# Performance work log

Measured on AMD Instinct MI355X. Metric: run time of the kernel, lower is better.

The kernel has to match this reference:

```python
import jax, jax.numpy as jnp
import numpy as np

N = 16384
D = 256


def setup_inputs() -> dict:
    key = jax.random.key(0)
    k1, k2, k3, k4 = jax.random.split(key, 4)
    x = jax.random.normal(k1, (N, D), dtype=jnp.float32)
    adj = jax.random.randint(k2, (N, N), 0, 2, dtype=jnp.int32)  # dense 0/1 adjacency
    W = jax.random.normal(k3, (D, D), dtype=jnp.float32) * 0.05
    b = jax.random.normal(k4, (D,), dtype=jnp.float32) * 0.05
    return {"x": x, "adj": adj, "W": W, "b": b}


def reference(x, adj, W, b):
    # neighbors of node i are columns where adj[i, :] == 1; mean-aggregate then Linear
    a = (adj == 1).astype(x.dtype)               # [N, N]
    deg = jnp.sum(a, axis=1, keepdims=True)      # [N, 1]
    agg = jnp.einsum('ij,jf->if', a, x) / deg    # mean over neighbors, [N, D]
    return agg @ W.T + b                         # nn.Linear(in, out)
```

## Files before the change

kernel.cpp:

```cpp
#include <hip/hip_runtime.h>
#include <stdint.h>

typedef __attribute__((ext_vector_type(8))) short shortx8;
typedef __attribute__((ext_vector_type(4))) float floatx4;

#define NR 16384
#define DD 256
#define SA 72
#define KCH 8192
#define BK 64
#define NIT (KCH / BK)

__device__ __forceinline__ unsigned short f2bf(float f) {
    union { float f; uint32_t u; } v; v.f = f;
    uint32_t u = v.u;
    return (unsigned short)((u + 0x7FFFu + ((u >> 16) & 1u)) >> 16);
}

__global__ __launch_bounds__(256) void k_xpose(const float* __restrict__ x,
                                               unsigned short* __restrict__ xT) {
    __shared__ unsigned short t[64][72];
    const int kb = blockIdx.x * 64;
    const int nb = blockIdx.y * 64;
    const int tid = threadIdx.x;
    const int lr = tid >> 4;
    const int lc = (tid & 15) * 4;
#pragma unroll
    for (int i = 0; i < 4; ++i) {
        const int k = kb + lr + 16 * i;
        const float4 v = *(const float4*)(x + (size_t)k * DD + nb + lc);
        t[lc + 0][lr + 16 * i] = f2bf(v.x);
        t[lc + 1][lr + 16 * i] = f2bf(v.y);
        t[lc + 2][lr + 16 * i] = f2bf(v.z);
        t[lc + 3][lr + 16 * i] = f2bf(v.w);
    }
    __syncthreads();
#pragma unroll
    for (int i = 0; i < 4; ++i) {
        const int nl = lr + 16 * i;
        ushort4 o;
        o.x = t[nl][lc + 0]; o.y = t[nl][lc + 1];
        o.z = t[nl][lc + 2]; o.w = t[nl][lc + 3];
        *(ushort4*)(xT + (size_t)(nb + nl) * NR + kb + lc) = o;
    }
}

__global__ __launch_bounds__(256, 2) void k_agg(const int* __restrict__ adj,
                                                const unsigned short* __restrict__ xT,
                                                float* __restrict__ aggP,
                                                float* __restrict__ degP) {
    __shared__ __align__(16) unsigned short As[64 * SA];
    __shared__ __align__(16) unsigned short Bs[256 * SA];
    __shared__ int degs[64];

    const int tid  = threadIdx.x;
    const int wave = tid >> 6;
    const int lane = tid & 63;
    const int q    = lane >> 4;
    const int ln   = lane & 15;
    const int m0   = blockIdx.x * 64;
    const int kb0  = blockIdx.y * KCH;

    if (tid < 64) degs[tid] = 0;

    const int arow = tid >> 4;
    const int acol = (tid & 15) * 4;

    const int* ap0 = adj + (size_t)(m0 + arow) * NR + kb0 + acol;
    const int* ap1 = ap0 + (size_t)16 * NR;
    const int* ap2 = ap0 + (size_t)32 * NR;
    const int* ap3 = ap0 + (size_t)48 * NR;

    const unsigned short* bg[9];
    unsigned short* const blb = Bs + wave * 9 * 512;
#pragma unroll
    for (int j = 0; j < 9; ++j) {
        const int cid = (wave * 9 + j) * 64 + lane;
        const int n = cid / 9;
        int c = cid - n * 9; if (c > 7) c = 7;
        bg[j] = xT + (size_t)n * NR + kb0 + c * 8;
    }

    floatx4 acc[4][4] = {};
    int dacc0 = 0, dacc1 = 0, dacc2 = 0, dacc3 = 0;

    for (int it = 0; it < NIT; ++it) {
        __syncthreads();

#pragma unroll
        for (int j = 0; j < 9; ++j) {
            __builtin_amdgcn_global_load_lds(
                (const __attribute__((address_space(1))) void*)bg[j],
                (__attribute__((address_space(3))) void*)(blb + j * 512),
                16, 0, 0);
            bg[j] += BK;
        }

        const int4 a0 = *(const int4*)ap0; ap0 += BK;
        const int4 a1 = *(const int4*)ap1; ap1 += BK;
        const int4 a2 = *(const int4*)ap2; ap2 += BK;
        const int4 a3 = *(const int4*)ap3; ap3 += BK;

        ushort4 w;
        w.x = a0.x ? 0x3F80 : 0; w.y = a0.y ? 0x3F80 : 0;
        w.z = a0.z ? 0x3F80 : 0; w.w = a0.w ? 0x3F80 : 0;
        *(ushort4*)&As[(arow +  0) * SA + acol] = w;
        dacc0 += a0.x + a0.y + a0.z + a0.w;

        w.x = a1.x ? 0x3F80 : 0; w.y = a1.y ? 0x3F80 : 0;
        w.z = a1.z ? 0x3F80 : 0; w.w = a1.w ? 0x3F80 : 0;
        *(ushort4*)&As[(arow + 16) * SA + acol] = w;
        dacc1 += a1.x + a1.y + a1.z + a1.w;

        w.x = a2.x ? 0x3F80 : 0; w.y = a2.y ? 0x3F80 : 0;
        w.z = a2.z ? 0x3F80 : 0; w.w = a2.w ? 0x3F80 : 0;
        *(ushort4*)&As[(arow + 32) * SA + acol] = w;
        dacc2 += a2.x + a2.y + a2.z + a2.w;

        w.x = a3.x ? 0x3F80 : 0; w.y = a3.y ? 0x3F80 : 0;
        w.z = a3.z ? 0x3F80 : 0; w.w = a3.w ? 0x3F80 : 0;
        *(ushort4*)&As[(arow + 48) * SA + acol] = w;
        dacc3 += a3.x + a3.y + a3.z + a3.w;

        __syncthreads();

#pragma unroll
        for (int ks = 0; ks < 2; ++ks) {
            const int kk = ks * 32 + q * 8;
            shortx8 af[4], bf[4];
#pragma unroll
            for (int mt = 0; mt < 4; ++mt)
                af[mt] = *(const shortx8*)&As[(mt * 16 + ln) * SA + kk];
#pragma unroll
            for (int nt = 0; nt < 4; ++nt)
                bf[nt] = *(const shortx8*)&Bs[(wave * 64 + nt * 16 + ln) * SA + kk];
#pragma unroll
            for (int mt = 0; mt < 4; ++mt)
#pragma unroll
                for (int nt = 0; nt < 4; ++nt)
                    acc[mt][nt] = __builtin_amdgcn_mfma_f32_16x16x32_bf16(
                        af[mt], bf[nt], acc[mt][nt], 0, 0, 0);
        }
    }

    atomicAdd(&degs[arow +  0], dacc0);
    atomicAdd(&degs[arow + 16], dacc1);
    atomicAdd(&degs[arow + 32], dacc2);
    atomicAdd(&degs[arow + 48], dacc3);
    __syncthreads();
    if (tid < 64) degP[(size_t)blockIdx.y * NR + m0 + tid] = (float)degs[tid];

    float* const outb = aggP + (size_t)blockIdx.y * NR * DD;
#pragma unroll
    for (int mt = 0; mt < 4; ++mt)
#pragma unroll
        for (int nt = 0; nt < 4; ++nt)
#pragma unroll
            for (int r = 0; r < 4; ++r) {
                const int row = m0 + mt * 16 + q * 4 + r;
                const int col = wave * 64 + nt * 16 + ln;
                outb[(size_t)row * DD + col] = acc[mt][nt][r];
            }
}

__global__ __launch_bounds__(256, 2) void k_lin(const float* __restrict__ aggP,
                                                const float* __restrict__ degP,
                                                const float* __restrict__ W,
                                                const float* __restrict__ bias,
                                                float* __restrict__ out) {
    __shared__ __align__(16) unsigned short As[64 * SA];
    __shared__ __align__(16) unsigned short Bs[256 * SA];
    __shared__ float rdeg[64];
    __shared__ float bsh[256];

    const int tid  = threadIdx.x;
    const int wave = tid >> 6;
    const int lane = tid & 63;
    const int q    = lane >> 4;
    const int ln   = lane & 15;
    const int m0   = blockIdx.x * 64;

    if (tid < 64) {
        const float d = degP[m0 + tid] + degP[NR + m0 + tid];
        rdeg[tid] = 1.0f / d;
    }
    bsh[tid] = bias[tid];

    const int arow = tid >> 4;
    const int acol = (tid & 15) * 4;

    floatx4 acc[4][4] = {};

    for (int it = 0; it < 4; ++it) {
        const int kb = it * 64;
        __syncthreads();

#pragma unroll
        for (int i = 0; i < 4; ++i) {
            const int r = arow + 16 * i;
            const size_t g = (size_t)(m0 + r) * DD + kb + acol;
            const float4 p0 = *(const float4*)(aggP + g);
            const float4 p1 = *(const float4*)(aggP + (size_t)NR * DD + g);
            const float s = rdeg[r];
            ushort4 o;
            o.x = f2bf((p0.x + p1.x) * s);
            o.y = f2bf((p0.y + p1.y) * s);
            o.z = f2bf((p0.z + p1.z) * s);
            o.w = f2bf((p0.w + p1.w) * s);
            *(ushort4*)&As[r * SA + acol] = o;
        }
#pragma unroll
        for (int i = 0; i < 16; ++i) {
            const int r = arow + 16 * i;
            const float4 w4 = *(const float4*)(W + (size_t)r * DD + kb + acol);
            ushort4 o;
            o.x = f2bf(w4.x); o.y = f2bf(w4.y);
            o.z = f2bf(w4.z); o.w = f2bf(w4.w);
            *(ushort4*)&Bs[r * SA + acol] = o;
        }
        __syncthreads();

#pragma unroll
        for (int ks = 0; ks < 2; ++ks) {
            const int kk = ks * 32 + q * 8;
            shortx8 af[4], bf[4];
#pragma unroll
            for (int mt = 0; mt < 4; ++mt)
                af[mt] = *(const shortx8*)&As[(mt * 16 + ln) * SA + kk];
#pragma unroll
            for (int nt = 0; nt < 4; ++nt)
                bf[nt] = *(const shortx8*)&Bs[(wave * 64 + nt * 16 + ln) * SA + kk];
#pragma unroll
            for (int mt = 0; mt < 4; ++mt)
#pragma unroll
                for (int nt = 0; nt < 4; ++nt)
                    acc[mt][nt] = __builtin_amdgcn_mfma_f32_16x16x32_bf16(
                        af[mt], bf[nt], acc[mt][nt], 0, 0, 0);
        }
    }

#pragma unroll
    for (int mt = 0; mt < 4; ++mt)
#pragma unroll
        for (int nt = 0; nt < 4; ++nt)
#pragma unroll
            for (int r = 0; r < 4; ++r) {
                const int row = m0 + mt * 16 + q * 4 + r;
                const int col = wave * 64 + nt * 16 + ln;
                out[(size_t)row * DD + col] = acc[mt][nt][r] + bsh[col];
            }
}

extern "C" void kernel_launch(void* const* d_in, const int* in_sizes, int n_in,
                              void* d_out, int out_size, void* d_ws, size_t ws_size,
                              hipStream_t stream) {
    const float* x    = (const float*)d_in[0];
    const int*   adj  = (const int*)d_in[1];
    const float* W    = (const float*)d_in[2];
    const float* bias = (const float*)d_in[3];
    float* out = (float*)d_out;

    unsigned short* xT  = (unsigned short*)d_ws;
    float* aggP = (float*)((char*)d_ws + (size_t)8 * 1024 * 1024);
    float* degP = (float*)((char*)d_ws + (size_t)40 * 1024 * 1024);

    k_xpose<<<dim3(NR / 64, DD / 64), 256, 0, stream>>>(x, xT);
    k_agg<<<dim3(NR / 64, 2), 256, 0, stream>>>(adj, xT, aggP, degP);
    k_lin<<<dim3(NR / 64), 256, 0, stream>>>(aggP, degP, W, bias, out);
}
```

Before: 1.586 ms.

## Split aggregation K into four chunks and prefetch adjacency loads into registers

Raises the split-K factor of the aggregation GEMM from 2 to 4, giving more blocks to fill the GPU, and raises the launch-bounds occupancy hint to 3 blocks per CU. The adjacency int4 loads for the next tile are now issued right after the barrier, before the MFMA compute, so the global-load latency overlaps the math. The linear kernel sums four partial aggregates and degrees instead of two. This adds partial-sum traffic and workspace, and more register pressure under the tighter occupancy bound.

```diff
diff --git a/kernel.cpp b/kernel.cpp
--- a/kernel.cpp
+++ b/kernel.cpp
@@ -7,7 +7,8 @@
 #define NR 16384
 #define DD 256
 #define SA 72
-#define KCH 8192
+#define NSPLIT 4
+#define KCH (NR / NSPLIT)
 #define BK 64
 #define NIT (KCH / BK)
 
@@ -45,7 +46,7 @@
     }
 }
 
-__global__ __launch_bounds__(256, 2) void k_agg(const int* __restrict__ adj,
+__global__ __launch_bounds__(256, 3) void k_agg(const int* __restrict__ adj,
                                                 const unsigned short* __restrict__ xT,
                                                 float* __restrict__ aggP,
                                                 float* __restrict__ degP) {
@@ -84,6 +85,11 @@
     floatx4 acc[4][4] = {};
     int dacc0 = 0, dacc1 = 0, dacc2 = 0, dacc3 = 0;
 
+    int4 a0 = *(const int4*)ap0;
+    int4 a1 = *(const int4*)ap1;
+    int4 a2 = *(const int4*)ap2;
+    int4 a3 = *(const int4*)ap3;
+
     for (int it = 0; it < NIT; ++it) {
         __syncthreads();
 
@@ -96,11 +102,6 @@
             bg[j] += BK;
         }
 
-        const int4 a0 = *(const int4*)ap0; ap0 += BK;
-        const int4 a1 = *(const int4*)ap1; ap1 += BK;
-        const int4 a2 = *(const int4*)ap2; ap2 += BK;
-        const int4 a3 = *(const int4*)ap3; ap3 += BK;
-
         ushort4 w;
         w.x = a0.x ? 0x3F80 : 0; w.y = a0.y ? 0x3F80 : 0;
         w.z = a0.z ? 0x3F80 : 0; w.w = a0.w ? 0x3F80 : 0;
@@ -123,6 +124,14 @@
         dacc3 += a3.x + a3.y + a3.z + a3.w;
 
         __syncthreads();
+
+        if (it + 1 < NIT) {
+            ap0 += BK; ap1 += BK; ap2 += BK; ap3 += BK;
+            a0 = *(const int4*)ap0;
+            a1 = *(const int4*)ap1;
+            a2 = *(const int4*)ap2;
+            a3 = *(const int4*)ap3;
+        }
 
 #pragma unroll
         for (int ks = 0; ks < 2; ++ks) {
@@ -181,7 +190,9 @@
     const int m0   = blockIdx.x * 64;
 
     if (tid < 64) {
-        const float d = degP[m0 + tid] + degP[NR + m0 + tid];
+        float d = 0.f;
+#pragma unroll
+        for (int s = 0; s < NSPLIT; ++s) d += degP[(size_t)s * NR + m0 + tid];
         rdeg[tid] = 1.0f / d;
     }
     bsh[tid] = bias[tid];
@@ -199,14 +210,18 @@
         for (int i = 0; i < 4; ++i) {
             const int r = arow + 16 * i;
             const size_t g = (size_t)(m0 + r) * DD + kb + acol;
-            const float4 p0 = *(const float4*)(aggP + g);
-            const float4 p1 = *(const float4*)(aggP + (size_t)NR * DD + g);
-            const float s = rdeg[r];
+            float4 p = *(const float4*)(aggP + g);
+#pragma unroll
+            for (int s = 1; s < NSPLIT; ++s) {
+                const float4 ps = *(const float4*)(aggP + (size_t)s * NR * DD + g);
+                p.x += ps.x; p.y += ps.y; p.z += ps.z; p.w += ps.w;
+            }
+            const float sc = rdeg[r];
             ushort4 o;
-            o.x = f2bf((p0.x + p1.x) * s);
-            o.y = f2bf((p0.y + p1.y) * s);
-            o.z = f2bf((p0.z + p1.z) * s);
-            o.w = f2bf((p0.w + p1.w) * s);
+            o.x = f2bf(p.x * sc);
+            o.y = f2bf(p.y * sc);
+            o.z = f2bf(p.z * sc);
+            o.w = f2bf(p.w * sc);
             *(ushort4*)&As[r * SA + acol] = o;
         }
 #pragma unroll
@@ -262,9 +277,9 @@
 
     unsigned short* xT  = (unsigned short*)d_ws;
     float* aggP = (float*)((char*)d_ws + (size_t)8 * 1024 * 1024);
-    float* degP = (float*)((char*)d_ws + (size_t)40 * 1024 * 1024);
+    float* degP = (float*)((char*)d_ws + (size_t)(8 + 16 * NSPLIT) * 1024 * 1024);
 
     k_xpose<<<dim3(NR / 64, DD / 64), 256, 0, stream>>>(x, xT);
-    k_agg<<<dim3(NR / 64, 2), 256, 0, stream>>>(adj, xT, aggP, degP);
+    k_agg<<<dim3(NR / 64, NSPLIT), 256, 0, stream>>>(adj, xT, aggP, degP);
     k_lin<<<dim3(NR / 64), 256, 0, stream>>>(aggP, degP, W, bias, out);
 }
```

Result: faster. 1.528 ms (-3.6%).
